# Optimization experiments

Hardware: AMD Instinct MI355X
Metric: run time of the kernel (lower is better)

Reference implementation:

```python
import jax, jax.numpy as jnp
import numpy as np

EMBED = 1024
HEADS = 16
HEAD_DIM = EMBED // HEADS
B, S = 2, 2048


def setup_inputs() -> dict:
    key = jax.random.key(0)
    ks = jax.random.split(key, 9)
    std = 1.0 / np.sqrt(EMBED)
    mk = lambda k: jax.random.uniform(k, (EMBED, EMBED), jnp.float32, -std, std)
    bk = lambda k: jax.random.uniform(k, (EMBED,), jnp.float32, -std, std)
    return {
        "x": jax.random.normal(ks[0], (B, S, EMBED), jnp.float32),
        "Wq": mk(ks[1]), "bq": bk(ks[2]),
        "Wk": mk(ks[3]), "bk": bk(ks[4]),
        "Wv": mk(ks[5]), "bv": bk(ks[6]),
        "Wo": mk(ks[7]), "bo": bk(ks[8]),
    }


def reference(x, Wq, bq, Wk, bk, Wv, bv, Wo, bo):
    b, s, _ = x.shape
    scale = HEAD_DIM ** -0.5
    # Linear layers: y = x @ W^T + b (torch nn.Linear convention)
    def heads(W, bias):
        y = jnp.einsum('bse,fe->bsf', x, W) + bias
        return y.reshape(b, s, HEADS, HEAD_DIM).transpose(0, 2, 1, 3)  # [b,h,s,d]
    Q, K, V = heads(Wq, bq), heads(Wk, bk), heads(Wv, bv)
    scores = jnp.einsum('bhqd,bhkd->bhqk', Q, K) * scale
    attn = jax.nn.softmax(scores, axis=-1)
    out = jnp.einsum('bhqk,bhkd->bhqd', attn, V)
    out = out.transpose(0, 2, 1, 3).reshape(b, s, EMBED)
    return jnp.einsum('bse,fe->bsf', out, Wo) + bo
```

## Files before the change

kernel.cpp:

```cpp
#include <hip/hip_runtime.h>
#include <hip/hip_bf16.h>
#include <cstddef>

#define SEQ   2048
#define EMB   1024
#define NHEAD 16
#define HDIM  64
#define BATCH 2
#define MROWS (BATCH * SEQ)
#define BH_STRIDE (SEQ * HDIM)
#define CSC_F 0.180336874f

typedef __attribute__((ext_vector_type(8))) short frag_ab;
typedef __attribute__((ext_vector_type(4))) float frag_cd;

#define GLOBAL_AS __attribute__((address_space(1)))
#define LDS_AS    __attribute__((address_space(3)))

__device__ __forceinline__ unsigned short f2bf(float f) {
    unsigned u = __float_as_uint(f);
    u += 0x7FFF + ((u >> 16) & 1);
    return (unsigned short)(u >> 16);
}
__device__ __forceinline__ unsigned short f2bf_trunc(float f) {
    return (unsigned short)(__float_as_uint(f) >> 16);
}
__device__ __forceinline__ void gld16(const unsigned short* g, unsigned short* l) {
    __builtin_amdgcn_global_load_lds((GLOBAL_AS const unsigned int*)g,
                                     (LDS_AS unsigned int*)l, 16, 0, 0);
}

__global__ __launch_bounds__(256) void cvt_all(const float* __restrict__ x,
                                               const float* __restrict__ Wq,
                                               const float* __restrict__ Wk,
                                               const float* __restrict__ Wv,
                                               unsigned short* __restrict__ xb,
                                               unsigned short* __restrict__ wqkv) {
    size_t e = ((size_t)blockIdx.x * 256 + threadIdx.x) * 8;
    const float* s;
    unsigned short* d;
    float sc = 1.0f;
    const size_t NX = (size_t)MROWS * EMB;
    const size_t NW = (size_t)EMB * EMB;
    if (e < NX) { s = x + e; d = xb + e; }
    else if (e < NX + NW)     { s = Wq + (e - NX);          d = wqkv + (e - NX); sc = CSC_F; }
    else if (e < NX + 2 * NW) { s = Wk + (e - NX - NW);     d = wqkv + (e - NX); }
    else                      { s = Wv + (e - NX - 2 * NW); d = wqkv + (e - NX); }
    float4 f0 = *(const float4*)s;
    float4 f1 = *(const float4*)(s + 4);
    ushort4 lo, hi;
    lo.x = f2bf(f0.x * sc); lo.y = f2bf(f0.y * sc); lo.z = f2bf(f0.z * sc); lo.w = f2bf(f0.w * sc);
    hi.x = f2bf(f1.x * sc); hi.y = f2bf(f1.y * sc); hi.z = f2bf(f1.z * sc); hi.w = f2bf(f1.w * sc);
    *(ushort4*)d = lo;
    *(ushort4*)(d + 4) = hi;
}

__global__ __launch_bounds__(256) void cvt_bf16(const float* __restrict__ s,
                                                unsigned short* __restrict__ d, int n) {
    int i = (blockIdx.x * 256 + threadIdx.x) * 8;
    if (i >= n) return;
    float4 f0 = *(const float4*)&s[i];
    float4 f1 = *(const float4*)&s[i + 4];
    ushort4 lo, hi;
    lo.x = f2bf(f0.x); lo.y = f2bf(f0.y); lo.z = f2bf(f0.z); lo.w = f2bf(f0.w);
    hi.x = f2bf(f1.x); hi.y = f2bf(f1.y); hi.z = f2bf(f1.z); hi.w = f2bf(f1.w);
    *(ushort4*)&d[i] = lo;
    *(ushort4*)&d[i + 4] = hi;
}

template <bool QKV, int BN>
__global__ __launch_bounds__(256, 3) void gemm128(const unsigned short* __restrict__ A,
                                                  const unsigned short* __restrict__ W0,
                                                  const unsigned short* __restrict__ W1,
                                                  const unsigned short* __restrict__ W2,
                                                  const float* __restrict__ b0,
                                                  const float* __restrict__ b1,
                                                  const float* __restrict__ b2,
                                                  void* __restrict__ o0,
                                                  void* __restrict__ o1,
                                                  void* __restrict__ o2) {
    constexpr int K = EMB;
    constexpr int NTC = BN / 32;
    __shared__ __align__(16) unsigned short SB[8192 + BN * 64];
    unsigned short* As = SB;
    unsigned short* Bs = SB + 8192;

    const int bidx = blockIdx.x;
    const int g8 = bidx & 7, t = bidx >> 3;
    const int my = g8 * 4 + (t & 3);
    const int mx = QKV ? ((t >> 2) & 7) : (t >> 2);
    const int z = QKV ? (t >> 5) : 0;

    const unsigned short* W = (z == 0) ? W0 : (z == 1) ? W1 : W2;
    const float* bias = (z == 0) ? b0 : (z == 1) ? b1 : b2;
    void* outv = (z == 0) ? o0 : (z == 1) ? o1 : o2;

    const int m0 = my * 128;
    const int n0 = mx * BN;
    const int tid = threadIdx.x;
    const int lane = tid & 63, w = tid >> 6;
    const int wr = w >> 1, wc = w & 1;
    const int lm = lane & 15, lq = lane >> 4;

    const int cs = (((tid & 7) ^ ((tid >> 3) & 7)) << 3);
    const int sx = lm & 7;

    frag_cd acc[4][NTC];
#pragma unroll
    for (int mt = 0; mt < 4; ++mt)
#pragma unroll
        for (int nt = 0; nt < NTC; ++nt) acc[mt][nt] = (frag_cd){0.f, 0.f, 0.f, 0.f};

    for (int k0 = 0; k0 < K; k0 += 64) {
#pragma unroll
        for (int it = 0; it < 4; ++it) {
            int flat = (it * 256 + tid) * 8;
            int r = flat >> 6;
            gld16(&A[(size_t)(m0 + r) * K + k0 + cs], &As[flat]);
        }
#pragma unroll
        for (int it = 0; it < BN / 32; ++it) {
            int flat = (it * 256 + tid) * 8;
            int r = flat >> 6;
            gld16(&W[(size_t)(n0 + r) * K + k0 + cs], &Bs[flat]);
        }
        __syncthreads();

#pragma unroll
        for (int kk = 0; kk < 2; ++kk) {
            frag_ab af[4], bf[NTC];
#pragma unroll
            for (int mt = 0; mt < 4; ++mt)
                af[mt] = *(const frag_ab*)&As[(wr * 64 + mt * 16 + lm) * 64
                                              + (((kk * 4 + lq) ^ sx) << 3)];
#pragma unroll
            for (int nt = 0; nt < NTC; ++nt)
                bf[nt] = *(const frag_ab*)&Bs[(wc * (BN / 2) + nt * 16 + lm) * 64
                                              + (((kk * 4 + lq) ^ sx) << 3)];
#pragma unroll
            for (int mt = 0; mt < 4; ++mt)
#pragma unroll
                for (int nt = 0; nt < NTC; ++nt)
                    acc[mt][nt] = __builtin_amdgcn_mfma_f32_16x16x32_bf16(
                        af[mt], bf[nt], acc[mt][nt], 0, 0, 0);
        }
        __syncthreads();
    }

    if constexpr (!QKV) {
#pragma unroll
        for (int mt = 0; mt < 4; ++mt)
#pragma unroll
            for (int nt = 0; nt < NTC; ++nt) {
                int col = n0 + wc * (BN / 2) + nt * 16 + lm;
                float bv = bias[col];
#pragma unroll
                for (int r = 0; r < 4; ++r) {
                    int row = m0 + wr * 64 + mt * 16 + lq * 4 + r;
                    ((float*)outv)[(size_t)row * EMB + col] = acc[mt][nt][r] + bv;
                }
            }
    } else {
        const float bscale = (z == 0) ? CSC_F : 1.0f;
#pragma unroll
        for (int mt = 0; mt < 4; ++mt)
#pragma unroll
            for (int nt = 0; nt < NTC; ++nt) {
                int col = n0 + wc * 64 + nt * 16 + lm;
                float bv = bias[col] * bscale;
#pragma unroll
                for (int r = 0; r < 4; ++r) {
                    unsigned short o = f2bf(acc[mt][nt][r] + bv);
                    int l, pos;
                    if (z < 2) {
                        l = wc * 16 + (wr * 4 + mt) * 2 + (nt >> 1);
                        pos = ((nt * 2 + (lm >> 3)) & 3) * 128 + (lq * 4 + r) * 8 + (lm & 7);
                    } else {
                        l = wc * 16 + (wr * 2 + (mt >> 1)) * 4 + nt;
                        pos = ((mt & 1) * 2 + (lq >> 1)) * 128 + lm * 8 + (lq & 1) * 4 + r;
                    }
                    SB[l * 512 + pos] = o;
                }
            }
        __syncthreads();

        unsigned short* out = (unsigned short*)outv;
        const int b = m0 >> 11;
        const int hb = n0 >> 6;
        const int sg16 = (m0 & (SEQ - 1)) >> 4;
        const int sb32 = (m0 & (SEQ - 1)) >> 5;
#pragma unroll
        for (int it = 0; it < 8; ++it) {
            int cl = it * 4 + w;
            uint4 v = *(const uint4*)&SB[cl * 512 + lane * 8];
            size_t chunk;
            if (z < 2) {
                int h = cl >> 4, sg = (cl >> 1) & 7, dh = cl & 1;
                chunk = ((size_t)(b * NHEAD + hb + h) * 128 + sg16 + sg) * 2 + dh;
            } else {
                int h = cl >> 4, sb = (cl >> 2) & 3, dq = cl & 3;
                chunk = ((size_t)(b * NHEAD + hb + h) * 64 + sb32 + sb) * 4 + dq;
            }
            *(uint4*)&out[chunk * 512 + lane * 8] = v;
        }
    }
}

#define PSTRIDE 72
#define CSTRIDE 81

__global__ __launch_bounds__(256, 2) void attn_fused(const unsigned short* __restrict__ Q,
                                                     const unsigned short* __restrict__ Kf,
                                                     const unsigned short* __restrict__ Vf,
                                                     unsigned short* __restrict__ O) {
    const int bidx = blockIdx.x;
    const int g8 = bidx & 7, t = bidx >> 3;
    const int bh = g8 * 4 + (t & 3);
    const int qt = t >> 2;
    const int w = threadIdx.x >> 6, lane = threadIdx.x & 63;
    const int lm = lane & 15, lq = lane >> 4;
    const int qs = w & 1;
    const int kh = w >> 1;

    __shared__ __align__(16) unsigned char SMEM[2 * 64 * CSTRIDE * 4 * sizeof(float) / 4];
    unsigned short* P = (unsigned short*)SMEM;

    const unsigned short* Qb = Q + (size_t)bh * BH_STRIDE;
    const unsigned short* Kb = Kf + (size_t)bh * BH_STRIDE;
    const unsigned short* Vb = Vf + (size_t)bh * BH_STRIDE;

    const int ga = qt * 8 + qs * 4;
    frag_ab qf[4][2];
#pragma unroll
    for (int qi = 0; qi < 4; ++qi) {
        qf[qi][0] = *(const frag_ab*)&Qb[(((ga + qi) * 2 + 0) * 64 + lane) * 8];
        qf[qi][1] = *(const frag_ab*)&Qb[(((ga + qi) * 2 + 1) * 64 + lane) * 8];
    }

    frag_ab vone;
#pragma unroll
    for (int j = 0; j < 8; ++j) vone[j] = (short)0x3F80;

    frag_cd oa[4][4], oc[4];
#pragma unroll
    for (int qi = 0; qi < 4; ++qi) {
        oc[qi] = (frag_cd){0.f, 0.f, 0.f, 0.f};
#pragma unroll
        for (int dt = 0; dt < 4; ++dt) oa[qi][dt] = (frag_cd){0.f, 0.f, 0.f, 0.f};
    }

    unsigned short* Pw = &P[w * (64 * PSTRIDE)];
    const frag_cd z = (frag_cd){0.f, 0.f, 0.f, 0.f};

    const int j_base = kh * (SEQ / 2);
    for (int jj = 0; jj < SEQ / 2; jj += 64) {
        const int j = j_base + jj;
        const int kg = j >> 4, jb = j >> 5;

        frag_ab kc[4][2], vc[2][4];
#pragma unroll
        for (int c = 0; c < 4; ++c) {
            kc[c][0] = *(const frag_ab*)&Kb[(((kg + c) * 2 + 0) * 64 + lane) * 8];
            kc[c][1] = *(const frag_ab*)&Kb[(((kg + c) * 2 + 1) * 64 + lane) * 8];
        }
#pragma unroll
        for (int j2 = 0; j2 < 2; ++j2)
#pragma unroll
            for (int dt = 0; dt < 4; ++dt)
                vc[j2][dt] = *(const frag_ab*)&Vb[(((jb + j2) * 4 + dt) * 64 + lane) * 8];

#pragma unroll
        for (int c = 0; c < 4; ++c) {
#pragma unroll
            for (int qi = 0; qi < 4; ++qi) {
                frag_cd sc = __builtin_amdgcn_mfma_f32_16x16x32_bf16(qf[qi][0], kc[c][0], z, 0, 0, 0);
                sc = __builtin_amdgcn_mfma_f32_16x16x32_bf16(qf[qi][1], kc[c][1], sc, 0, 0, 0);
#pragma unroll
                for (int r = 0; r < 4; ++r) {
                    float p = __builtin_amdgcn_exp2f(sc[r]);
                    Pw[(qi * 16 + lq * 4 + r) * PSTRIDE + c * 16 + lm] = f2bf_trunc(p);
                }
            }
        }

#pragma unroll
        for (int qi = 0; qi < 4; ++qi) {
            frag_ab pf0 = *(const frag_ab*)&Pw[(qi * 16 + lm) * PSTRIDE + lq * 8];
            frag_ab pf1 = *(const frag_ab*)&Pw[(qi * 16 + lm) * PSTRIDE + 32 + lq * 8];
            oc[qi] = __builtin_amdgcn_mfma_f32_16x16x32_bf16(pf0, vone, oc[qi], 0, 0, 0);
            oc[qi] = __builtin_amdgcn_mfma_f32_16x16x32_bf16(pf1, vone, oc[qi], 0, 0, 0);
#pragma unroll
            for (int dt = 0; dt < 4; ++dt) {
                oa[qi][dt] = __builtin_amdgcn_mfma_f32_16x16x32_bf16(pf0, vc[0][dt], oa[qi][dt], 0, 0, 0);
                oa[qi][dt] = __builtin_amdgcn_mfma_f32_16x16x32_bf16(pf1, vc[1][dt], oa[qi][dt], 0, 0, 0);
            }
        }
    }

    __syncthreads();
    float* C = (float*)SMEM;
    if (w >= 2) {
        float* dst = C + (size_t)(w - 2) * (64 * CSTRIDE) + lane * CSTRIDE;
        int idx = 0;
#pragma unroll
        for (int qi = 0; qi < 4; ++qi)
#pragma unroll
            for (int dt = 0; dt < 4; ++dt)
#pragma unroll
                for (int r = 0; r < 4; ++r) dst[idx++] = oa[qi][dt][r];
#pragma unroll
        for (int qi = 0; qi < 4; ++qi)
#pragma unroll
            for (int r = 0; r < 4; ++r) dst[idx++] = oc[qi][r];
    }
    __syncthreads();
    if (w < 2) {
        const float* src = C + (size_t)w * (64 * CSTRIDE) + lane * CSTRIDE;
        int idx = 0;
#pragma unroll
        for (int qi = 0; qi < 4; ++qi)
#pragma unroll
            for (int dt = 0; dt < 4; ++dt)
#pragma unroll
                for (int r = 0; r < 4; ++r) oa[qi][dt][r] += src[idx++];
#pragma unroll
        for (int qi = 0; qi < 4; ++qi)
#pragma unroll
            for (int r = 0; r < 4; ++r) oc[qi][r] += src[idx++];

        const int b = bh >> 4, h = bh & (NHEAD - 1);
#pragma unroll
        for (int qi = 0; qi < 4; ++qi) {
            const int q0 = (ga + qi) * 16;
#pragma unroll
            for (int r = 0; r < 4; ++r) {
                float inv = 1.0f / oc[qi][r];
                int srow = q0 + lq * 4 + r;
#pragma unroll
                for (int dt = 0; dt < 4; ++dt) {
                    int d = dt * 16 + lm;
                    O[((size_t)(b * SEQ + srow)) * EMB + h * HDIM + d] = f2bf(oa[qi][dt][r] * inv);
                }
            }
        }
    }
}

extern "C" void kernel_launch(void* const* d_in, const int* in_sizes, int n_in,
                              void* d_out, int out_size, void* d_ws, size_t ws_size,
                              hipStream_t stream) {
    const float* x  = (const float*)d_in[0];
    const float* Wq = (const float*)d_in[1];
    const float* bq = (const float*)d_in[2];
    const float* Wk = (const float*)d_in[3];
    const float* bk = (const float*)d_in[4];
    const float* Wv = (const float*)d_in[5];
    const float* bv = (const float*)d_in[6];
    const float* Wo = (const float*)d_in[7];
    const float* bo = (const float*)d_in[8];

    unsigned short* xb    = (unsigned short*)d_ws;
    unsigned short* q_ws  = xb + (size_t)MROWS * EMB;
    unsigned short* k_ws  = q_ws + (size_t)MROWS * EMB;
    unsigned short* vt_ws = k_ws + (size_t)MROWS * EMB;
    unsigned short* o_ws  = xb;
    unsigned short* wqkv  = (unsigned short*)d_out;
    unsigned short* wo_b  = q_ws;

    dim3 blk(256);
    cvt_all<<<dim3((MROWS * EMB + 3 * EMB * EMB) / 2048), blk, 0, stream>>>(
        x, Wq, Wk, Wv, xb, wqkv);

    gemm128<true, 128><<<dim3(768), blk, 0, stream>>>(
        xb, wqkv, wqkv + EMB * EMB, wqkv + 2 * EMB * EMB,
        bq, bk, bv, q_ws, k_ws, vt_ws);

    attn_fused<<<dim3(512), blk, 0, stream>>>(q_ws, k_ws, vt_ws, o_ws);

    cvt_bf16<<<dim3(EMB * EMB / 2048), blk, 0, stream>>>(Wo, wo_b, EMB * EMB);
    gemm128<false, 64><<<dim3(512), blk, 0, stream>>>(
        o_ws, wo_b, wo_b, wo_b, bo, bo, bo, d_out, d_out, d_out);
}
```

Before: 183.6 us.

## Fuse all stages into one persistent kernel with software grid barriers

Replaces the five separate launches (convert, QKV GEMM, attention, Wo convert, output GEMM) with a single persistent kernel of 512 blocks that runs each stage in turn and separates them with atomic-counter grid barriers. The intent is to remove launch overhead and the tail gaps between kernels. The cost is that all 512 blocks must be co-resident for the spin barriers to work, the QKV GEMM now runs as 768 tiles over 512 blocks (two waves), and an extra memset is added. The old multi-kernel path is kept as a fallback when the workspace is too small for the barrier counters.

```diff
diff --git a/kernel.cpp b/kernel.cpp
--- a/kernel.cpp
+++ b/kernel.cpp
@@ -28,6 +28,356 @@
 __device__ __forceinline__ void gld16(const unsigned short* g, unsigned short* l) {
     __builtin_amdgcn_global_load_lds((GLOBAL_AS const unsigned int*)g,
                                      (LDS_AS unsigned int*)l, 16, 0, 0);
+}
+__device__ __forceinline__ void cvt8(const float* __restrict__ s,
+                                     unsigned short* __restrict__ d, float sc) {
+    float4 f0 = *(const float4*)s;
+    float4 f1 = *(const float4*)(s + 4);
+    ushort4 lo, hi;
+    lo.x = f2bf(f0.x * sc); lo.y = f2bf(f0.y * sc); lo.z = f2bf(f0.z * sc); lo.w = f2bf(f0.w * sc);
+    hi.x = f2bf(f1.x * sc); hi.y = f2bf(f1.y * sc); hi.z = f2bf(f1.z * sc); hi.w = f2bf(f1.w * sc);
+    *(ushort4*)d = lo;
+    *(ushort4*)(d + 4) = hi;
+}
+
+__device__ __forceinline__ void grid_barrier(unsigned* __restrict__ cnt,
+                                             unsigned target) {
+    __syncthreads();
+    if (threadIdx.x == 0) {
+        __threadfence();
+        atomicAdd(cnt, 1u);
+        unsigned iters = 0;
+        while (atomicAdd(cnt, 0u) < target) {
+            __builtin_amdgcn_s_sleep(8);
+            if (++iters > 100000000u) break;
+        }
+        __threadfence();
+    }
+    __syncthreads();
+}
+
+template <bool QKV, int BN>
+__device__ __forceinline__ void gemm_body(int lb, unsigned short* __restrict__ SB,
+                                          const unsigned short* __restrict__ A,
+                                          const unsigned short* __restrict__ W0,
+                                          const unsigned short* __restrict__ W1,
+                                          const unsigned short* __restrict__ W2,
+                                          const float* __restrict__ b0,
+                                          const float* __restrict__ b1,
+                                          const float* __restrict__ b2,
+                                          void* __restrict__ o0,
+                                          void* __restrict__ o1,
+                                          void* __restrict__ o2) {
+    constexpr int K = EMB;
+    constexpr int NTC = BN / 32;
+    unsigned short* As = SB;
+    unsigned short* Bs = SB + 8192;
+
+    const int g8 = lb & 7, t = lb >> 3;
+    const int my = g8 * 4 + (t & 3);
+    const int mx = QKV ? ((t >> 2) & 7) : (t >> 2);
+    const int z = QKV ? (t >> 5) : 0;
+
+    const unsigned short* W = (z == 0) ? W0 : (z == 1) ? W1 : W2;
+    const float* bias = (z == 0) ? b0 : (z == 1) ? b1 : b2;
+    void* outv = (z == 0) ? o0 : (z == 1) ? o1 : o2;
+
+    const int m0 = my * 128;
+    const int n0 = mx * BN;
+    const int tid = threadIdx.x;
+    const int lane = tid & 63, w = tid >> 6;
+    const int wr = w >> 1, wc = w & 1;
+    const int lm = lane & 15, lq = lane >> 4;
+
+    const int cs = (((tid & 7) ^ ((tid >> 3) & 7)) << 3);
+    const int sx = lm & 7;
+
+    frag_cd acc[4][NTC];
+#pragma unroll
+    for (int mt = 0; mt < 4; ++mt)
+#pragma unroll
+        for (int nt = 0; nt < NTC; ++nt) acc[mt][nt] = (frag_cd){0.f, 0.f, 0.f, 0.f};
+
+    for (int k0 = 0; k0 < K; k0 += 64) {
+#pragma unroll
+        for (int it = 0; it < 4; ++it) {
+            int flat = (it * 256 + tid) * 8;
+            int r = flat >> 6;
+            gld16(&A[(size_t)(m0 + r) * K + k0 + cs], &As[flat]);
+        }
+#pragma unroll
+        for (int it = 0; it < BN / 32; ++it) {
+            int flat = (it * 256 + tid) * 8;
+            int r = flat >> 6;
+            gld16(&W[(size_t)(n0 + r) * K + k0 + cs], &Bs[flat]);
+        }
+        __syncthreads();
+
+#pragma unroll
+        for (int kk = 0; kk < 2; ++kk) {
+            frag_ab af[4], bf[NTC];
+#pragma unroll
+            for (int mt = 0; mt < 4; ++mt)
+                af[mt] = *(const frag_ab*)&As[(wr * 64 + mt * 16 + lm) * 64
+                                              + (((kk * 4 + lq) ^ sx) << 3)];
+#pragma unroll
+            for (int nt = 0; nt < NTC; ++nt)
+                bf[nt] = *(const frag_ab*)&Bs[(wc * (BN / 2) + nt * 16 + lm) * 64
+                                              + (((kk * 4 + lq) ^ sx) << 3)];
+#pragma unroll
+            for (int mt = 0; mt < 4; ++mt)
+#pragma unroll
+                for (int nt = 0; nt < NTC; ++nt)
+                    acc[mt][nt] = __builtin_amdgcn_mfma_f32_16x16x32_bf16(
+                        af[mt], bf[nt], acc[mt][nt], 0, 0, 0);
+        }
+        __syncthreads();
+    }
+
+    if constexpr (!QKV) {
+#pragma unroll
+        for (int mt = 0; mt < 4; ++mt)
+#pragma unroll
+            for (int nt = 0; nt < NTC; ++nt) {
+                int col = n0 + wc * (BN / 2) + nt * 16 + lm;
+                float bv = bias[col];
+#pragma unroll
+                for (int r = 0; r < 4; ++r) {
+                    int row = m0 + wr * 64 + mt * 16 + lq * 4 + r;
+                    ((float*)outv)[(size_t)row * EMB + col] = acc[mt][nt][r] + bv;
+                }
+            }
+    } else {
+        const float bscale = (z == 0) ? CSC_F : 1.0f;
+#pragma unroll
+        for (int mt = 0; mt < 4; ++mt)
+#pragma unroll
+            for (int nt = 0; nt < NTC; ++nt) {
+                int col = n0 + wc * 64 + nt * 16 + lm;
+                float bv = bias[col] * bscale;
+#pragma unroll
+                for (int r = 0; r < 4; ++r) {
+                    unsigned short o = f2bf(acc[mt][nt][r] + bv);
+                    int l, pos;
+                    if (z < 2) {
+                        l = wc * 16 + (wr * 4 + mt) * 2 + (nt >> 1);
+                        pos = ((nt * 2 + (lm >> 3)) & 3) * 128 + (lq * 4 + r) * 8 + (lm & 7);
+                    } else {
+                        l = wc * 16 + (wr * 2 + (mt >> 1)) * 4 + nt;
+                        pos = ((mt & 1) * 2 + (lq >> 1)) * 128 + lm * 8 + (lq & 1) * 4 + r;
+                    }
+                    SB[l * 512 + pos] = o;
+                }
+            }
+        __syncthreads();
+
+        unsigned short* out = (unsigned short*)outv;
+        const int b = m0 >> 11;
+        const int hb = n0 >> 6;
+        const int sg16 = (m0 & (SEQ - 1)) >> 4;
+        const int sb32 = (m0 & (SEQ - 1)) >> 5;
+#pragma unroll
+        for (int it = 0; it < 8; ++it) {
+            int cl = it * 4 + w;
+            uint4 v = *(const uint4*)&SB[cl * 512 + lane * 8];
+            size_t chunk;
+            if (z < 2) {
+                int h = cl >> 4, sg = (cl >> 1) & 7, dh = cl & 1;
+                chunk = ((size_t)(b * NHEAD + hb + h) * 128 + sg16 + sg) * 2 + dh;
+            } else {
+                int h = cl >> 4, sb = (cl >> 2) & 3, dq = cl & 3;
+                chunk = ((size_t)(b * NHEAD + hb + h) * 64 + sb32 + sb) * 4 + dq;
+            }
+            *(uint4*)&out[chunk * 512 + lane * 8] = v;
+        }
+    }
+    __syncthreads();
+}
+
+#define PSTRIDE 72
+#define CSTRIDE 81
+#define SMEM_BYTES (2 * 64 * CSTRIDE * 4)
+
+__device__ __forceinline__ void attn_body(int bidx, unsigned char* __restrict__ SMEM,
+                                          const unsigned short* __restrict__ Q,
+                                          const unsigned short* __restrict__ Kf,
+                                          const unsigned short* __restrict__ Vf,
+                                          unsigned short* __restrict__ O) {
+    const int g8 = bidx & 7, t = bidx >> 3;
+    const int bh = g8 * 4 + (t & 3);
+    const int qt = t >> 2;
+    const int w = threadIdx.x >> 6, lane = threadIdx.x & 63;
+    const int lm = lane & 15, lq = lane >> 4;
+    const int qs = w & 1;
+    const int kh = w >> 1;
+
+    unsigned short* P = (unsigned short*)SMEM;
+
+    const unsigned short* Qb = Q + (size_t)bh * BH_STRIDE;
+    const unsigned short* Kb = Kf + (size_t)bh * BH_STRIDE;
+    const unsigned short* Vb = Vf + (size_t)bh * BH_STRIDE;
+
+    const int ga = qt * 8 + qs * 4;
+    frag_ab qf[4][2];
+#pragma unroll
+    for (int qi = 0; qi < 4; ++qi) {
+        qf[qi][0] = *(const frag_ab*)&Qb[(((ga + qi) * 2 + 0) * 64 + lane) * 8];
+        qf[qi][1] = *(const frag_ab*)&Qb[(((ga + qi) * 2 + 1) * 64 + lane) * 8];
+    }
+
+    frag_ab vone;
+#pragma unroll
+    for (int j = 0; j < 8; ++j) vone[j] = (short)0x3F80;
+
+    frag_cd oa[4][4], oc[4];
+#pragma unroll
+    for (int qi = 0; qi < 4; ++qi) {
+        oc[qi] = (frag_cd){0.f, 0.f, 0.f, 0.f};
+#pragma unroll
+        for (int dt = 0; dt < 4; ++dt) oa[qi][dt] = (frag_cd){0.f, 0.f, 0.f, 0.f};
+    }
+
+    unsigned short* Pw = &P[w * (64 * PSTRIDE)];
+    const frag_cd z = (frag_cd){0.f, 0.f, 0.f, 0.f};
+
+    const int j_base = kh * (SEQ / 2);
+    for (int jj = 0; jj < SEQ / 2; jj += 64) {
+        const int j = j_base + jj;
+        const int kg = j >> 4, jb = j >> 5;
+
+        frag_ab kc[4][2], vc[2][4];
+#pragma unroll
+        for (int c = 0; c < 4; ++c) {
+            kc[c][0] = *(const frag_ab*)&Kb[(((kg + c) * 2 + 0) * 64 + lane) * 8];
+            kc[c][1] = *(const frag_ab*)&Kb[(((kg + c) * 2 + 1) * 64 + lane) * 8];
+        }
+#pragma unroll
+        for (int j2 = 0; j2 < 2; ++j2)
+#pragma unroll
+            for (int dt = 0; dt < 4; ++dt)
+                vc[j2][dt] = *(const frag_ab*)&Vb[(((jb + j2) * 4 + dt) * 64 + lane) * 8];
+
+#pragma unroll
+        for (int c = 0; c < 4; ++c) {
+#pragma unroll
+            for (int qi = 0; qi < 4; ++qi) {
+                frag_cd sc = __builtin_amdgcn_mfma_f32_16x16x32_bf16(qf[qi][0], kc[c][0], z, 0, 0, 0);
+                sc = __builtin_amdgcn_mfma_f32_16x16x32_bf16(qf[qi][1], kc[c][1], sc, 0, 0, 0);
+#pragma unroll
+                for (int r = 0; r < 4; ++r) {
+                    float p = __builtin_amdgcn_exp2f(sc[r]);
+                    Pw[(qi * 16 + lq * 4 + r) * PSTRIDE + c * 16 + lm] = f2bf_trunc(p);
+                }
+            }
+        }
+
+#pragma unroll
+        for (int qi = 0; qi < 4; ++qi) {
+            frag_ab pf0 = *(const frag_ab*)&Pw[(qi * 16 + lm) * PSTRIDE + lq * 8];
+            frag_ab pf1 = *(const frag_ab*)&Pw[(qi * 16 + lm) * PSTRIDE + 32 + lq * 8];
+            oc[qi] = __builtin_amdgcn_mfma_f32_16x16x32_bf16(pf0, vone, oc[qi], 0, 0, 0);
+            oc[qi] = __builtin_amdgcn_mfma_f32_16x16x32_bf16(pf1, vone, oc[qi], 0, 0, 0);
+#pragma unroll
+            for (int dt = 0; dt < 4; ++dt) {
+                oa[qi][dt] = __builtin_amdgcn_mfma_f32_16x16x32_bf16(pf0, vc[0][dt], oa[qi][dt], 0, 0, 0);
+                oa[qi][dt] = __builtin_amdgcn_mfma_f32_16x16x32_bf16(pf1, vc[1][dt], oa[qi][dt], 0, 0, 0);
+            }
+        }
+    }
+
+    __syncthreads();
+    float* C = (float*)SMEM;
+    if (w >= 2) {
+        float* dst = C + (size_t)(w - 2) * (64 * CSTRIDE) + lane * CSTRIDE;
+        int idx = 0;
+#pragma unroll
+        for (int qi = 0; qi < 4; ++qi)
+#pragma unroll
+            for (int dt = 0; dt < 4; ++dt)
+#pragma unroll
+                for (int r = 0; r < 4; ++r) dst[idx++] = oa[qi][dt][r];
+#pragma unroll
+        for (int qi = 0; qi < 4; ++qi)
+#pragma unroll
+            for (int r = 0; r < 4; ++r) dst[idx++] = oc[qi][r];
+    }
+    __syncthreads();
+    if (w < 2) {
+        const float* src = C + (size_t)w * (64 * CSTRIDE) + lane * CSTRIDE;
+        int idx = 0;
+#pragma unroll
+        for (int qi = 0; qi < 4; ++qi)
+#pragma unroll
+            for (int dt = 0; dt < 4; ++dt)
+#pragma unroll
+                for (int r = 0; r < 4; ++r) oa[qi][dt][r] += src[idx++];
+#pragma unroll
+        for (int qi = 0; qi < 4; ++qi)
+#pragma unroll
+            for (int r = 0; r < 4; ++r) oc[qi][r] += src[idx++];
+
+        const int b = bh >> 4, h = bh & (NHEAD - 1);
+#pragma unroll
+        for (int qi = 0; qi < 4; ++qi) {
+            const int q0 = (ga + qi) * 16;
+#pragma unroll
+            for (int r = 0; r < 4; ++r) {
+                float inv = 1.0f / oc[qi][r];
+                int srow = q0 + lq * 4 + r;
+#pragma unroll
+                for (int dt = 0; dt < 4; ++dt) {
+                    int d = dt * 16 + lm;
+                    O[((size_t)(b * SEQ + srow)) * EMB + h * HDIM + d] = f2bf(oa[qi][dt][r] * inv);
+                }
+            }
+        }
+    }
+    __syncthreads();
+}
+
+__global__ __launch_bounds__(256, 2) void mha_fused(
+    const float* __restrict__ x,
+    const float* __restrict__ Wq, const float* __restrict__ bq,
+    const float* __restrict__ Wk, const float* __restrict__ bk,
+    const float* __restrict__ Wv, const float* __restrict__ bv,
+    const float* __restrict__ Wo, const float* __restrict__ bo,
+    float* __restrict__ out, unsigned short* __restrict__ ws,
+    unsigned* __restrict__ bar) {
+    __shared__ __align__(16) unsigned char SMEM[SMEM_BYTES];
+
+    unsigned short* xb    = ws;
+    unsigned short* q_ws  = ws + 1 * 4194304;
+    unsigned short* k_ws  = ws + 2 * 4194304;
+    unsigned short* vt_ws = ws + 3 * 4194304;
+    unsigned short* o_ws  = xb;
+    unsigned short* wqkv  = (unsigned short*)out;
+    unsigned short* wo_b  = q_ws;
+
+    const int gt = blockIdx.x * 256 + threadIdx.x;
+    const size_t base = (size_t)gt * 8;
+
+#pragma unroll
+    for (int i = 0; i < 4; ++i)
+        cvt8(x + (size_t)i * 1048576 + base, xb + (size_t)i * 1048576 + base, 1.0f);
+    cvt8(Wq + base, wqkv + base, CSC_F);
+    cvt8(Wk + base, wqkv + 1048576 + base, 1.0f);
+    cvt8(Wv + base, wqkv + 2097152 + base, 1.0f);
+    grid_barrier(bar + 0, 512);
+
+    for (int lb = blockIdx.x; lb < 768; lb += 512)
+        gemm_body<true, 128>(lb, (unsigned short*)SMEM, xb,
+                             wqkv, wqkv + 1048576, wqkv + 2097152,
+                             bq, bk, bv, q_ws, k_ws, vt_ws);
+    grid_barrier(bar + 1, 512);
+
+    attn_body(blockIdx.x, SMEM, q_ws, k_ws, vt_ws, o_ws);
+    grid_barrier(bar + 2, 512);
+
+    cvt8(Wo + base, wo_b + base, 1.0f);
+    grid_barrier(bar + 3, 512);
+
+    gemm_body<false, 64>(blockIdx.x, (unsigned short*)SMEM, o_ws,
+                         wo_b, wo_b, wo_b, bo, bo, bo, out, out, out);
 }
 
 __global__ __launch_bounds__(256) void cvt_all(const float* __restrict__ x,
@@ -46,26 +396,14 @@
     else if (e < NX + NW)     { s = Wq + (e - NX);          d = wqkv + (e - NX); sc = CSC_F; }
     else if (e < NX + 2 * NW) { s = Wk + (e - NX - NW);     d = wqkv + (e - NX); }
     else                      { s = Wv + (e - NX - 2 * NW); d = wqkv + (e - NX); }
-    float4 f0 = *(const float4*)s;
-    float4 f1 = *(const float4*)(s + 4);
-    ushort4 lo, hi;
-    lo.x = f2bf(f0.x * sc); lo.y = f2bf(f0.y * sc); lo.z = f2bf(f0.z * sc); lo.w = f2bf(f0.w * sc);
-    hi.x = f2bf(f1.x * sc); hi.y = f2bf(f1.y * sc); hi.z = f2bf(f1.z * sc); hi.w = f2bf(f1.w * sc);
-    *(ushort4*)d = lo;
-    *(ushort4*)(d + 4) = hi;
+    cvt8(s, d, sc);
 }
 
 __global__ __launch_bounds__(256) void cvt_bf16(const float* __restrict__ s,
                                                 unsigned short* __restrict__ d, int n) {
     int i = (blockIdx.x * 256 + threadIdx.x) * 8;
     if (i >= n) return;
-    float4 f0 = *(const float4*)&s[i];
-    float4 f1 = *(const float4*)&s[i + 4];
-    ushort4 lo, hi;
-    lo.x = f2bf(f0.x); lo.y = f2bf(f0.y); lo.z = f2bf(f0.z); lo.w = f2bf(f0.w);
-    hi.x = f2bf(f1.x); hi.y = f2bf(f1.y); hi.z = f2bf(f1.z); hi.w = f2bf(f1.w);
-    *(ushort4*)&d[i] = lo;
-    *(ushort4*)&d[i + 4] = hi;
+    cvt8(s + i, d + i, 1.0f);
 }
 
 template <bool QKV, int BN>
@@ -79,271 +417,16 @@
                                                   void* __restrict__ o0,
                                                   void* __restrict__ o1,
                                                   void* __restrict__ o2) {
-    constexpr int K = EMB;
-    constexpr int NTC = BN / 32;
     __shared__ __align__(16) unsigned short SB[8192 + BN * 64];
-    unsigned short* As = SB;
-    unsigned short* Bs = SB + 8192;
-
-    const int bidx = blockIdx.x;
-    const int g8 = bidx & 7, t = bidx >> 3;
-    const int my = g8 * 4 + (t & 3);
-    const int mx = QKV ? ((t >> 2) & 7) : (t >> 2);
-    const int z = QKV ? (t >> 5) : 0;
-
-    const unsigned short* W = (z == 0) ? W0 : (z == 1) ? W1 : W2;
-    const float* bias = (z == 0) ? b0 : (z == 1) ? b1 : b2;
-    void* outv = (z == 0) ? o0 : (z == 1) ? o1 : o2;
-
-    const int m0 = my * 128;
-    const int n0 = mx * BN;
-    const int tid = threadIdx.x;
-    const int lane = tid & 63, w = tid >> 6;
-    const int wr = w >> 1, wc = w & 1;
-    const int lm = lane & 15, lq = lane >> 4;
-
-    const int cs = (((tid & 7) ^ ((tid >> 3) & 7)) << 3);
-    const int sx = lm & 7;
-
-    frag_cd acc[4][NTC];
-#pragma unroll
-    for (int mt = 0; mt < 4; ++mt)
-#pragma unroll
-        for (int nt = 0; nt < NTC; ++nt) acc[mt][nt] = (frag_cd){0.f, 0.f, 0.f, 0.f};
-
-    for (int k0 = 0; k0 < K; k0 += 64) {
-#pragma unroll
-        for (int it = 0; it < 4; ++it) {
-            int flat = (it * 256 + tid) * 8;
-            int r = flat >> 6;
-            gld16(&A[(size_t)(m0 + r) * K + k0 + cs], &As[flat]);
-        }
-#pragma unroll
-        for (int it = 0; it < BN / 32; ++it) {
-            int flat = (it * 256 + tid) * 8;
-            int r = flat >> 6;
-            gld16(&W[(size_t)(n0 + r) * K + k0 + cs], &Bs[flat]);
-        }
-        __syncthreads();
-
-#pragma unroll
-        for (int kk = 0; kk < 2; ++kk) {
-            frag_ab af[4], bf[NTC];
-#pragma unroll
-            for (int mt = 0; mt < 4; ++mt)
-                af[mt] = *(const frag_ab*)&As[(wr * 64 + mt * 16 + lm) * 64
-                                              + (((kk * 4 + lq) ^ sx) << 3)];
-#pragma unroll
-            for (int nt = 0; nt < NTC; ++nt)
-                bf[nt] = *(const frag_ab*)&Bs[(wc * (BN / 2) + nt * 16 + lm) * 64
-                                              + (((kk * 4 + lq) ^ sx) << 3)];
-#pragma unroll
-            for (int mt = 0; mt < 4; ++mt)
-#pragma unroll
-                for (int nt = 0; nt < NTC; ++nt)
-                    acc[mt][nt] = __builtin_amdgcn_mfma_f32_16x16x32_bf16(
-                        af[mt], bf[nt], acc[mt][nt], 0, 0, 0);
-        }
-        __syncthreads();
-    }
-
-    if constexpr (!QKV) {
-#pragma unroll
-        for (int mt = 0; mt < 4; ++mt)
-#pragma unroll
-            for (int nt = 0; nt < NTC; ++nt) {
-                int col = n0 + wc * (BN / 2) + nt * 16 + lm;
-                float bv = bias[col];
-#pragma unroll
-                for (int r = 0; r < 4; ++r) {
-                    int row = m0 + wr * 64 + mt * 16 + lq * 4 + r;
-                    ((float*)outv)[(size_t)row * EMB + col] = acc[mt][nt][r] + bv;
-                }
-            }
-    } else {
-        const float bscale = (z == 0) ? CSC_F : 1.0f;
-#pragma unroll
-        for (int mt = 0; mt < 4; ++mt)
-#pragma unroll
-            for (int nt = 0; nt < NTC; ++nt) {
-                int col = n0 + wc * 64 + nt * 16 + lm;
-                float bv = bias[col] * bscale;
-#pragma unroll
-                for (int r = 0; r < 4; ++r) {
-                    unsigned short o = f2bf(acc[mt][nt][r] + bv);
-                    int l, pos;
-                    if (z < 2) {
-                        l = wc * 16 + (wr * 4 + mt) * 2 + (nt >> 1);
-                        pos = ((nt * 2 + (lm >> 3)) & 3) * 128 + (lq * 4 + r) * 8 + (lm & 7);
-                    } else {
-                        l = wc * 16 + (wr * 2 + (mt >> 1)) * 4 + nt;
-                        pos = ((mt & 1) * 2 + (lq >> 1)) * 128 + lm * 8 + (lq & 1) * 4 + r;
-                    }
-                    SB[l * 512 + pos] = o;
-                }
-            }
-        __syncthreads();
-
-        unsigned short* out = (unsigned short*)outv;
-        const int b = m0 >> 11;
-        const int hb = n0 >> 6;
-        const int sg16 = (m0 & (SEQ - 1)) >> 4;
-        const int sb32 = (m0 & (SEQ - 1)) >> 5;
-#pragma unroll
-        for (int it = 0; it < 8; ++it) {
-            int cl = it * 4 + w;
-            uint4 v = *(const uint4*)&SB[cl * 512 + lane * 8];
-            size_t chunk;
-            if (z < 2) {
-                int h = cl >> 4, sg = (cl >> 1) & 7, dh = cl & 1;
-                chunk = ((size_t)(b * NHEAD + hb + h) * 128 + sg16 + sg) * 2 + dh;
-            } else {
-                int h = cl >> 4, sb = (cl >> 2) & 3, dq = cl & 3;
-                chunk = ((size_t)(b * NHEAD + hb + h) * 64 + sb32 + sb) * 4 + dq;
-            }
-            *(uint4*)&out[chunk * 512 + lane * 8] = v;
-        }
-    }
-}
-
-#define PSTRIDE 72
-#define CSTRIDE 81
+    gemm_body<QKV, BN>(blockIdx.x, SB, A, W0, W1, W2, b0, b1, b2, o0, o1, o2);
+}
 
 __global__ __launch_bounds__(256, 2) void attn_fused(const unsigned short* __restrict__ Q,
                                                      const unsigned short* __restrict__ Kf,
                                                      const unsigned short* __restrict__ Vf,
                                                      unsigned short* __restrict__ O) {
-    const int bidx = blockIdx.x;
-    const int g8 = bidx & 7, t = bidx >> 3;
-    const int bh = g8 * 4 + (t & 3);
-    const int qt = t >> 2;
-    const int w = threadIdx.x >> 6, lane = threadIdx.x & 63;
-    const int lm = lane & 15, lq = lane >> 4;
-    const int qs = w & 1;
-    const int kh = w >> 1;
-
-    __shared__ __align__(16) unsigned char SMEM[2 * 64 * CSTRIDE * 4 * sizeof(float) / 4];
-    unsigned short* P = (unsigned short*)SMEM;
-
-    const unsigned short* Qb = Q + (size_t)bh * BH_STRIDE;
-    const unsigned short* Kb = Kf + (size_t)bh * BH_STRIDE;
-    const unsigned short* Vb = Vf + (size_t)bh * BH_STRIDE;
-
-    const int ga = qt * 8 + qs * 4;
-    frag_ab qf[4][2];
-#pragma unroll
-    for (int qi = 0; qi < 4; ++qi) {
-        qf[qi][0] = *(const frag_ab*)&Qb[(((ga + qi) * 2 + 0) * 64 + lane) * 8];
-        qf[qi][1] = *(const frag_ab*)&Qb[(((ga + qi) * 2 + 1) * 64 + lane) * 8];
-    }
-
-    frag_ab vone;
-#pragma unroll
-    for (int j = 0; j < 8; ++j) vone[j] = (short)0x3F80;
-
-    frag_cd oa[4][4], oc[4];
-#pragma unroll
-    for (int qi = 0; qi < 4; ++qi) {
-        oc[qi] = (frag_cd){0.f, 0.f, 0.f, 0.f};
-#pragma unroll
-        for (int dt = 0; dt < 4; ++dt) oa[qi][dt] = (frag_cd){0.f, 0.f, 0.f, 0.f};
-    }
-
-    unsigned short* Pw = &P[w * (64 * PSTRIDE)];
-    const frag_cd z = (frag_cd){0.f, 0.f, 0.f, 0.f};
-
-    const int j_base = kh * (SEQ / 2);
-    for (int jj = 0; jj < SEQ / 2; jj += 64) {
-        const int j = j_base + jj;
-        const int kg = j >> 4, jb = j >> 5;
-
-        frag_ab kc[4][2], vc[2][4];
-#pragma unroll
-        for (int c = 0; c < 4; ++c) {
-            kc[c][0] = *(const frag_ab*)&Kb[(((kg + c) * 2 + 0) * 64 + lane) * 8];
-            kc[c][1] = *(const frag_ab*)&Kb[(((kg + c) * 2 + 1) * 64 + lane) * 8];
-        }
-#pragma unroll
-        for (int j2 = 0; j2 < 2; ++j2)
-#pragma unroll
-            for (int dt = 0; dt < 4; ++dt)
-                vc[j2][dt] = *(const frag_ab*)&Vb[(((jb + j2) * 4 + dt) * 64 + lane) * 8];
-
-#pragma unroll
-        for (int c = 0; c < 4; ++c) {
-#pragma unroll
-            for (int qi = 0; qi < 4; ++qi) {
-                frag_cd sc = __builtin_amdgcn_mfma_f32_16x16x32_bf16(qf[qi][0], kc[c][0], z, 0, 0, 0);
-                sc = __builtin_amdgcn_mfma_f32_16x16x32_bf16(qf[qi][1], kc[c][1], sc, 0, 0, 0);
-#pragma unroll
-                for (int r = 0; r < 4; ++r) {
-                    float p = __builtin_amdgcn_exp2f(sc[r]);
-                    Pw[(qi * 16 + lq * 4 + r) * PSTRIDE + c * 16 + lm] = f2bf_trunc(p);
-                }
-            }
-        }
-
-#pragma unroll
-        for (int qi = 0; qi < 4; ++qi) {
-            frag_ab pf0 = *(const frag_ab*)&Pw[(qi * 16 + lm) * PSTRIDE + lq * 8];
-            frag_ab pf1 = *(const frag_ab*)&Pw[(qi * 16 + lm) * PSTRIDE + 32 + lq * 8];
-            oc[qi] = __builtin_amdgcn_mfma_f32_16x16x32_bf16(pf0, vone, oc[qi], 0, 0, 0);
-            oc[qi] = __builtin_amdgcn_mfma_f32_16x16x32_bf16(pf1, vone, oc[qi], 0, 0, 0);
-#pragma unroll
-            for (int dt = 0; dt < 4; ++dt) {
-                oa[qi][dt] = __builtin_amdgcn_mfma_f32_16x16x32_bf16(pf0, vc[0][dt], oa[qi][dt], 0, 0, 0);
-                oa[qi][dt] = __builtin_amdgcn_mfma_f32_16x16x32_bf16(pf1, vc[1][dt], oa[qi][dt], 0, 0, 0);
-            }
-        }
-    }
-
-    __syncthreads();
-    float* C = (float*)SMEM;
-    if (w >= 2) {
-        float* dst = C + (size_t)(w - 2) * (64 * CSTRIDE) + lane * CSTRIDE;
-        int idx = 0;
-#pragma unroll
-        for (int qi = 0; qi < 4; ++qi)
-#pragma unroll
-            for (int dt = 0; dt < 4; ++dt)
-#pragma unroll
-                for (int r = 0; r < 4; ++r) dst[idx++] = oa[qi][dt][r];
-#pragma unroll
-        for (int qi = 0; qi < 4; ++qi)
-#pragma unroll
-            for (int r = 0; r < 4; ++r) dst[idx++] = oc[qi][r];
-    }
-    __syncthreads();
-    if (w < 2) {
-        const float* src = C + (size_t)w * (64 * CSTRIDE) + lane * CSTRIDE;
-        int idx = 0;
-#pragma unroll
-        for (int qi = 0; qi < 4; ++qi)
-#pragma unroll
-            for (int dt = 0; dt < 4; ++dt)
-#pragma unroll
-                for (int r = 0; r < 4; ++r) oa[qi][dt][r] += src[idx++];
-#pragma unroll
-        for (int qi = 0; qi < 4; ++qi)
-#pragma unroll
-            for (int r = 0; r < 4; ++r) oc[qi][r] += src[idx++];
-
-        const int b = bh >> 4, h = bh & (NHEAD - 1);
-#pragma unroll
-        for (int qi = 0; qi < 4; ++qi) {
-            const int q0 = (ga + qi) * 16;
-#pragma unroll
-            for (int r = 0; r < 4; ++r) {
-                float inv = 1.0f / oc[qi][r];
-                int srow = q0 + lq * 4 + r;
-#pragma unroll
-                for (int dt = 0; dt < 4; ++dt) {
-                    int d = dt * 16 + lm;
-                    O[((size_t)(b * SEQ + srow)) * EMB + h * HDIM + d] = f2bf(oa[qi][dt][r] * inv);
-                }
-            }
-        }
-    }
+    __shared__ __align__(16) unsigned char SMEM[SMEM_BYTES];
+    attn_body(blockIdx.x, SMEM, Q, Kf, Vf, O);
 }
 
 extern "C" void kernel_launch(void* const* d_in, const int* in_sizes, int n_in,
@@ -358,26 +441,34 @@
     const float* bv = (const float*)d_in[6];
     const float* Wo = (const float*)d_in[7];
     const float* bo = (const float*)d_in[8];
-
-    unsigned short* xb    = (unsigned short*)d_ws;
-    unsigned short* q_ws  = xb + (size_t)MROWS * EMB;
-    unsigned short* k_ws  = q_ws + (size_t)MROWS * EMB;
-    unsigned short* vt_ws = k_ws + (size_t)MROWS * EMB;
-    unsigned short* o_ws  = xb;
-    unsigned short* wqkv  = (unsigned short*)d_out;
-    unsigned short* wo_b  = q_ws;
-
-    dim3 blk(256);
-    cvt_all<<<dim3((MROWS * EMB + 3 * EMB * EMB) / 2048), blk, 0, stream>>>(
-        x, Wq, Wk, Wv, xb, wqkv);
-
-    gemm128<true, 128><<<dim3(768), blk, 0, stream>>>(
-        xb, wqkv, wqkv + EMB * EMB, wqkv + 2 * EMB * EMB,
-        bq, bk, bv, q_ws, k_ws, vt_ws);
-
-    attn_fused<<<dim3(512), blk, 0, stream>>>(q_ws, k_ws, vt_ws, o_ws);
-
-    cvt_bf16<<<dim3(EMB * EMB / 2048), blk, 0, stream>>>(Wo, wo_b, EMB * EMB);
-    gemm128<false, 64><<<dim3(512), blk, 0, stream>>>(
-        o_ws, wo_b, wo_b, wo_b, bo, bo, bo, d_out, d_out, d_out);
-}
+    float* out = (float*)d_out;
+    unsigned short* ws = (unsigned short*)d_ws;
+
+    const size_t WS_DATA = 4ull * 4194304ull * sizeof(unsigned short);
+
+    if (ws_size >= WS_DATA + 64) {
+        unsigned* bar = (unsigned*)((char*)d_ws + WS_DATA);
+        hipMemsetAsync(bar, 0, 4 * sizeof(unsigned), stream);
+        hipLaunchKernelGGL(mha_fused, dim3(512), dim3(256), 0, stream,
+                           x, Wq, bq, Wk, bk, Wv, bv, Wo, bo, out, ws, bar);
+    } else {
+        unsigned short* xb    = ws;
+        unsigned short* q_ws  = xb + (size_t)MROWS * EMB;
+        unsigned short* k_ws  = q_ws + (size_t)MROWS * EMB;
+        unsigned short* vt_ws = k_ws + (size_t)MROWS * EMB;
+        unsigned short* o_ws  = xb;
+        unsigned short* wqkv  = (unsigned short*)d_out;
+        unsigned short* wo_b  = q_ws;
+
+        dim3 blk(256);
+        cvt_all<<<dim3((MROWS * EMB + 3 * EMB * EMB) / 2048), blk, 0, stream>>>(
+            x, Wq, Wk, Wv, xb, wqkv);
+        gemm128<true, 128><<<dim3(768), blk, 0, stream>>>(
+            xb, wqkv, wqkv + EMB * EMB, wqkv + 2 * EMB * EMB,
+            bq, bk, bv, q_ws, k_ws, vt_ws);
+        attn_fused<<<dim3(512), blk, 0, stream>>>(q_ws, k_ws, vt_ws, o_ws);
+        cvt_bf16<<<dim3(EMB * EMB / 2048), blk, 0, stream>>>(Wo, wo_b, EMB * EMB);
+        gemm128<false, 64><<<dim3(512), blk, 0, stream>>>(
+            o_ws, wo_b, wo_b, wo_b, bo, bo, bo, d_out, d_out, d_out);
+    }
+}
```

New measurement: 402.4 us. +119.2%, slower.
